# Kernel tuning notes

Hardware: AMD Instinct MI355X
Metric: run time of the kernel (lower is better)

The kernel has to match this reference:

```python
import jax, jax.numpy as jnp
import numpy as np

TOP_K = 2
NUM_MOE_LAYERS = 12


def _gemma_mlp(x, gate_w, up_w, down_w):
    # GemmaMLP: down( gelu_tanh(gate(x)) * up(x) )
    g = jnp.einsum('bsh,hi->bsi', x, gate_w)
    u = jnp.einsum('bsh,hi->bsi', x, up_w)
    return jnp.einsum('bsi,ih->bsh', jax.nn.gelu(g, approximate=True) * u, down_w)


def setup_inputs() -> dict:
    key = jax.random.key(0)
    ks = jax.random.split(key, 8)
    B, S, H, I, E = 32, 256, 1024, 4096, 8  # batch, seq, hidden, intermediate, skill experts
    std = 0.02
    return {
        'x': jax.random.normal(ks[0], (B, S, H), jnp.float32),
        'router_logits': jax.random.normal(ks[1], (B, E), jnp.float32),
        'skill_gate': jax.random.normal(ks[2], (E, H, I), jnp.float32) * std,
        'skill_up': jax.random.normal(ks[3], (E, H, I), jnp.float32) * std,
        'skill_down': jax.random.normal(ks[4], (E, I, H), jnp.float32) * std,
        'shared_gate': jax.random.normal(ks[5], (H, I), jnp.float32) * std,
        'shared_up': jax.random.normal(ks[6], (H, I), jnp.float32) * std,
        'shared_down': jax.random.normal(ks[7], (I, H), jnp.float32) * std,
    }


def reference(x, router_logits, skill_gate, skill_up, skill_down,
              shared_gate, shared_up, shared_down):
    B = x.shape[0]
    E = skill_gate.shape[0]
    # top-k softmax routing (per sequence), renormalized over selected experts
    rw = jax.nn.softmax(router_logits.astype(jnp.float32), axis=-1)
    w, sel = jax.lax.top_k(rw, TOP_K)                      # [B, k]
    w = w / w.sum(axis=-1, keepdims=True)
    w = w.astype(x.dtype)
    # ScaleGradient: identity fwd, grad scaled by 1/num_moe_layers
    scale = 1.0 / NUM_MOE_LAYERS
    w = scale * w + (1.0 - scale) * jax.lax.stop_gradient(w)
    # dense combine weights [B, E]; zero weight == not routed (same math as gather/scatter)
    dense_w = jnp.zeros((B, E), x.dtype).at[jnp.arange(B)[:, None], sel].add(w)

    def step(acc, params):
        g, u, d, we = params                               # we: [B]
        return acc + we[:, None, None] * _gemma_mlp(x, g, u, d), None

    out, _ = jax.lax.scan(step, jnp.zeros_like(x),
                          (skill_gate, skill_up, skill_down, dense_w.T))
    out = out + _gemma_mlp(x, shared_gate, shared_up, shared_down)
    return out
```

## Files before the change

kernel.cpp:

```cpp
#include <hip/hip_runtime.h>

typedef __bf16 bf16x8 __attribute__((ext_vector_type(8)));
typedef float  f32x4  __attribute__((ext_vector_type(4)));

__device__ __forceinline__ unsigned short f2bf(float f) {
    unsigned u = __float_as_uint(f);
    u += 0x7fffu + ((u >> 16) & 1u);
    return (unsigned short)(u >> 16);
}

__device__ __forceinline__ void gld_lds16(const void* g, void* l) {
    __builtin_amdgcn_global_load_lds(
        (const __attribute__((address_space(1))) void*)g,
        (__attribute__((address_space(3))) void*)l,
        16, 0, 0);
}

#define NB  32
#define SQ  256
#define HD  1024
#define ID  4096
#define NEXP 8
#define PAIRS (NB * 3)

#define OFF_EID    ((size_t)0)
#define OFF_WGT    ((size_t)512)
#define OFF_XBF    ((size_t)1024)
#define OFF_GATET  (OFF_XBF   + (size_t)16777216)
#define OFF_UPT    (OFF_GATET + (size_t)75497472)
#define OFF_DOWNT  (OFF_UPT   + (size_t)75497472)
#define OFF_ACT    (OFF_DOWNT + (size_t)75497472)

__global__ void routing_kernel(const float* __restrict__ logits,
                               int* __restrict__ eid, float* __restrict__ wgt) {
    int b = threadIdx.x;
    if (b < NB) {
        float l[NEXP];
        for (int j = 0; j < NEXP; ++j) l[j] = logits[b * NEXP + j];
        int a0 = 0;
        for (int j = 1; j < NEXP; ++j) if (l[j] > l[a0]) a0 = j;
        int a1 = -1;
        for (int j = 0; j < NEXP; ++j) {
            if (j == a0) continue;
            if (a1 < 0 || l[j] > l[a1]) a1 = j;
        }
        float w0 = 1.0f / (1.0f + expf(l[a1] - l[a0]));
        eid[b * 3 + 0] = a0;  wgt[b * 3 + 0] = w0;
        eid[b * 3 + 1] = a1;  wgt[b * 3 + 1] = 1.0f - w0;
        eid[b * 3 + 2] = NEXP; wgt[b * 3 + 2] = 1.0f;
    }
}

__global__ void xcvt_kernel(const float* __restrict__ x,
                            unsigned short* __restrict__ xb, int n4) {
    int i = blockIdx.x * 256 + threadIdx.x;
    if (i < n4) {
        float4 v = ((const float4*)x)[i];
        union { unsigned short s[4]; uint2 u; } p;
        p.s[0] = f2bf(v.x); p.s[1] = f2bf(v.y);
        p.s[2] = f2bf(v.z); p.s[3] = f2bf(v.w);
        ((uint2*)xb)[i] = p.u;
    }
}

__global__ void transpose_cvt(const float* __restrict__ skill,
                              const float* __restrict__ shared_m,
                              unsigned short* __restrict__ out, int R, int C) {
    const int e = blockIdx.z;
    const float* src = (e < NEXP) ? (skill + (size_t)e * R * C) : shared_m;
    unsigned short* dst = out + (size_t)e * R * C;
    const int c0 = blockIdx.x * 64;
    const int r0 = blockIdx.y * 64;
    __shared__ unsigned short t[64][66];
    const int tid = threadIdx.x;
    const int lr = tid >> 4;
    const int lc = (tid & 15) * 4;
    for (int it = 0; it < 4; ++it) {
        int r = lr + it * 16;
        float4 v = *(const float4*)(src + (size_t)(r0 + r) * C + c0 + lc);
        t[r][lc + 0] = f2bf(v.x);
        t[r][lc + 1] = f2bf(v.y);
        t[r][lc + 2] = f2bf(v.z);
        t[r][lc + 3] = f2bf(v.w);
    }
    __syncthreads();
    const int oc = tid >> 2;
    const int k0 = (tid & 3) * 16;
    unsigned int pk[8];
    for (int j = 0; j < 8; ++j) {
        unsigned int lo = t[k0 + 2 * j + 0][oc];
        unsigned int hi = t[k0 + 2 * j + 1][oc];
        pk[j] = lo | (hi << 16);
    }
    unsigned short* dp = dst + (size_t)(c0 + oc) * R + r0 + k0;
    ((uint4*)dp)[0] = make_uint4(pk[0], pk[1], pk[2], pk[3]);
    ((uint4*)dp)[1] = make_uint4(pk[4], pk[5], pk[6], pk[7]);
}

__global__ __launch_bounds__(256, 2) void stage1_gateup(
    const unsigned short* __restrict__ xbf,
    const unsigned short* __restrict__ gateT,
    const unsigned short* __restrict__ upT,
    const int* __restrict__ eid, const float* __restrict__ wgt,
    unsigned short* __restrict__ act)
{
    const int nt = blockIdx.x;
    const int mt = blockIdx.y;
    const int p  = blockIdx.z;
    const int b  = p / 3;
    const int e  = eid[p];
    const float w = wgt[p];

    __shared__ __align__(16) unsigned short lds[3 * 128 * 64];
    unsigned short* La = lds;
    unsigned short* Lg = lds + 8192;
    unsigned short* Lu = lds + 16384;

    const int tid  = threadIdx.x;
    const int wave = tid >> 6;
    const int lane = tid & 63;
    const int wm = (wave >> 1) * 64;
    const int wn = (wave & 1) * 64;

    const unsigned short* Abase = xbf   + (size_t)(b * SQ + mt * 128) * HD;
    const unsigned short* Gbase = gateT + ((size_t)e * ID + nt * 128) * HD;
    const unsigned short* Ubase = upT   + ((size_t)e * ID + nt * 128) * HD;

    const int srow = lane >> 3;
    const int scol = (lane & 7) * 8;

    f32x4 accg[4][4], accu[4][4];
    for (int i = 0; i < 4; ++i)
        for (int j = 0; j < 4; ++j) { accg[i][j] = (f32x4)0.f; accu[i][j] = (f32x4)0.f; }

    const int lrow = lane & 15;
    const int kq   = (lane >> 4) * 8;

    for (int k0 = 0; k0 < HD; k0 += 64) {
        for (int q = 0; q < 4; ++q) {
            const int seg = wave * 4 + q;
            const size_t roff = (size_t)(seg * 8 + srow);
            gld_lds16(Abase + roff * HD + k0 + scol, La + seg * 512);
            gld_lds16(Gbase + roff * HD + k0 + scol, Lg + seg * 512);
            gld_lds16(Ubase + roff * HD + k0 + scol, Lu + seg * 512);
        }
        __syncthreads();
        for (int kk = 0; kk < 64; kk += 32) {
            bf16x8 af[4], gf[4], uf[4];
            for (int mf = 0; mf < 4; ++mf)
                af[mf] = *(const bf16x8*)(La + (wm + mf * 16 + lrow) * 64 + kk + kq);
            for (int nf = 0; nf < 4; ++nf) {
                gf[nf] = *(const bf16x8*)(Lg + (wn + nf * 16 + lrow) * 64 + kk + kq);
                uf[nf] = *(const bf16x8*)(Lu + (wn + nf * 16 + lrow) * 64 + kk + kq);
            }
            for (int mf = 0; mf < 4; ++mf)
                for (int nf = 0; nf < 4; ++nf) {
                    accg[mf][nf] = __builtin_amdgcn_mfma_f32_16x16x32_bf16(af[mf], gf[nf], accg[mf][nf], 0, 0, 0);
                    accu[mf][nf] = __builtin_amdgcn_mfma_f32_16x16x32_bf16(af[mf], uf[nf], accu[mf][nf], 0, 0, 0);
                }
        }
        __syncthreads();
    }

    unsigned short* actp = act + (size_t)p * (SQ * ID);
    const int rb = mt * 128 + wm + ((lane >> 4) << 2);
    const int cb = nt * 128 + wn + (lane & 15);
    for (int mf = 0; mf < 4; ++mf)
        for (int nf = 0; nf < 4; ++nf)
            for (int r = 0; r < 4; ++r) {
                float g = accg[mf][nf][r];
                float u = accu[mf][nf][r];
                float t = 0.7978845608028654f * (g + 0.044715f * g * g * g);
                float h = 0.5f * g * (1.0f + tanhf(t)) * u * w;
                actp[(size_t)(rb + mf * 16 + r) * ID + cb + nf * 16] = f2bf(h);
            }
}

__global__ __launch_bounds__(256, 2) void stage2_down(
    const unsigned short* __restrict__ act,
    const unsigned short* __restrict__ downT,
    const int* __restrict__ eid,
    float* __restrict__ out)
{
    const int nt = blockIdx.x;
    const int mt = blockIdx.y;
    const int b  = blockIdx.z;

    __shared__ __align__(16) unsigned short lds[2 * 128 * 64];
    unsigned short* La = lds;
    unsigned short* Lb = lds + 8192;

    const int tid  = threadIdx.x;
    const int wave = tid >> 6;
    const int lane = tid & 63;
    const int wm = (wave >> 1) * 64;
    const int wn = (wave & 1) * 64;

    const int e0 = eid[b * 3 + 0], e1 = eid[b * 3 + 1], e2 = eid[b * 3 + 2];

    const int srow = lane >> 3;
    const int scol = (lane & 7) * 8;
    const int lrow = lane & 15;
    const int kq   = (lane >> 4) * 8;

    f32x4 acc[4][4];
    for (int i = 0; i < 4; ++i)
        for (int j = 0; j < 4; ++j) acc[i][j] = (f32x4)0.f;

    for (int k0 = 0; k0 < 3 * ID; k0 += 64) {
        const int slot = k0 >> 12;
        const int i0   = k0 & (ID - 1);
        const int e    = (slot == 0) ? e0 : (slot == 1 ? e1 : e2);
        const unsigned short* Abase = act   + ((size_t)(b * 3 + slot) * SQ + mt * 128) * ID + i0;
        const unsigned short* Bbase = downT + ((size_t)e * HD + nt * 128) * ID + i0;
        for (int q = 0; q < 4; ++q) {
            const int seg = wave * 4 + q;
            const size_t roff = (size_t)(seg * 8 + srow);
            gld_lds16(Abase + roff * ID + scol, La + seg * 512);
            gld_lds16(Bbase + roff * ID + scol, Lb + seg * 512);
        }
        __syncthreads();
        for (int kk = 0; kk < 64; kk += 32) {
            bf16x8 af[4], bf[4];
            for (int mf = 0; mf < 4; ++mf)
                af[mf] = *(const bf16x8*)(La + (wm + mf * 16 + lrow) * 64 + kk + kq);
            for (int nf = 0; nf < 4; ++nf)
                bf[nf] = *(const bf16x8*)(Lb + (wn + nf * 16 + lrow) * 64 + kk + kq);
            for (int mf = 0; mf < 4; ++mf)
                for (int nf = 0; nf < 4; ++nf)
                    acc[mf][nf] = __builtin_amdgcn_mfma_f32_16x16x32_bf16(af[mf], bf[nf], acc[mf][nf], 0, 0, 0);
        }
        __syncthreads();
    }

    const int rb = mt * 128 + wm + ((lane >> 4) << 2);
    const int cb = nt * 128 + wn + (lane & 15);
    for (int mf = 0; mf < 4; ++mf)
        for (int nf = 0; nf < 4; ++nf)
            for (int r = 0; r < 4; ++r)
                out[((size_t)b * SQ + rb + mf * 16 + r) * HD + cb + nf * 16] = acc[mf][nf][r];
}

extern "C" void kernel_launch(void* const* d_in, const int* in_sizes, int n_in,
                              void* d_out, int out_size, void* d_ws, size_t ws_size,
                              hipStream_t stream) {
    const float* x        = (const float*)d_in[0];
    const float* logits   = (const float*)d_in[1];
    const float* sk_gate  = (const float*)d_in[2];
    const float* sk_up    = (const float*)d_in[3];
    const float* sk_down  = (const float*)d_in[4];
    const float* sh_gate  = (const float*)d_in[5];
    const float* sh_up    = (const float*)d_in[6];
    const float* sh_down  = (const float*)d_in[7];
    float* out = (float*)d_out;

    char* ws = (char*)d_ws;
    int*            eid   = (int*)(ws + OFF_EID);
    float*          wgt   = (float*)(ws + OFF_WGT);
    unsigned short* xbf   = (unsigned short*)(ws + OFF_XBF);
    unsigned short* gateT = (unsigned short*)(ws + OFF_GATET);
    unsigned short* upT   = (unsigned short*)(ws + OFF_UPT);
    unsigned short* downT = (unsigned short*)(ws + OFF_DOWNT);
    unsigned short* act   = (unsigned short*)(ws + OFF_ACT);

    routing_kernel<<<1, 64, 0, stream>>>(logits, eid, wgt);

    const int n4 = (NB * SQ * HD) / 4;
    xcvt_kernel<<<(n4 + 255) / 256, 256, 0, stream>>>(x, xbf, n4);

    transpose_cvt<<<dim3(ID / 64, HD / 64, 9), 256, 0, stream>>>(sk_gate, sh_gate, gateT, HD, ID);
    transpose_cvt<<<dim3(ID / 64, HD / 64, 9), 256, 0, stream>>>(sk_up,   sh_up,   upT,   HD, ID);
    transpose_cvt<<<dim3(HD / 64, ID / 64, 9), 256, 0, stream>>>(sk_down, sh_down, downT, ID, HD);

    stage1_gateup<<<dim3(ID / 128, SQ / 128, PAIRS), 256, 0, stream>>>(xbf, gateT, upT, eid, wgt, act);
    stage2_down<<<dim3(HD / 128, SQ / 128, NB), 256, 0, stream>>>(act, downT, eid, out);
}
```

Baseline: 1.307 ms.

## Rewrite MoE GEMMs with 256x128 tiles, swizzled LDS, double-buffered prefetch and split-K

Both GEMM kernels become 512-thread blocks. Stage 1 covers the full 256-row sequence per block, fusing the gate and up columns into one B tile. Blocks are ordered by expert through a sort table built in the routing kernel so same-expert tiles share cache. LDS is XOR-swizzled and double-buffered, with explicit vmcnt waits, sched barriers and raised priority around the MFMA bursts, and GELU now uses an exp-based form. Stage 2 uses 256x256 tiles with 2-way split-K into a partial buffer plus a combine kernel, which costs an extra full-output read/write pass in exchange for better occupancy and fewer blocks.

```diff
diff --git a/kernel.cpp b/kernel.cpp
--- a/kernel.cpp
+++ b/kernel.cpp
@@ -15,6 +15,10 @@
         (__attribute__((address_space(3))) void*)l,
         16, 0, 0);
 }
+
+#define WAITVM(N) asm volatile("s_waitcnt vmcnt(" #N ")" ::: "memory")
+#define SB0()     __builtin_amdgcn_sched_barrier(0)
+#define BAR()     __builtin_amdgcn_s_barrier()
 
 #define NB  32
 #define SQ  256
@@ -30,6 +34,8 @@
 #define OFF_UPT    (OFF_GATET + (size_t)75497472)
 #define OFF_DOWNT  (OFF_UPT   + (size_t)75497472)
 #define OFF_ACT    (OFF_DOWNT + (size_t)75497472)
+
+__device__ int d_sord[PAIRS];
 
 __global__ void routing_kernel(const float* __restrict__ logits,
                                int* __restrict__ eid, float* __restrict__ wgt) {
@@ -48,6 +54,14 @@
         eid[b * 3 + 0] = a0;  wgt[b * 3 + 0] = w0;
         eid[b * 3 + 1] = a1;  wgt[b * 3 + 1] = 1.0f - w0;
         eid[b * 3 + 2] = NEXP; wgt[b * 3 + 2] = 1.0f;
+    }
+    __syncthreads();
+    if (threadIdx.x == 0) {
+        int cnt[NEXP + 2];
+        for (int i = 0; i < NEXP + 2; ++i) cnt[i] = 0;
+        for (int i = 0; i < PAIRS; ++i) cnt[eid[i] + 1]++;
+        for (int e = 0; e < NEXP + 1; ++e) cnt[e + 1] += cnt[e];
+        for (int i = 0; i < PAIRS; ++i) d_sord[cnt[eid[i]]++] = i;
     }
 }
 
@@ -97,148 +111,273 @@
     ((uint4*)dp)[1] = make_uint4(pk[4], pk[5], pk[6], pk[7]);
 }
 
-__global__ __launch_bounds__(256, 2) void stage1_gateup(
+#define LDFRAGS(KH, MB)                                                      \
+    _Pragma("unroll") for (int i2 = 0; i2 < 4; ++i2)                         \
+        av[i2] = *(const bf16x8*)(Lc + (KH) + rdA + ((MB) + i2) * 512);
+#define LDBFRAGS(KH)                                                         \
+    _Pragma("unroll") for (int i2 = 0; i2 < 4; ++i2)                         \
+        bv[i2] = *(const bf16x8*)(Lc + (KH) + rdB + i2 * 512);
+#define DOMFMA(MB)                                                           \
+    __builtin_amdgcn_s_setprio(1);                                           \
+    _Pragma("unroll") for (int mi = 0; mi < 4; ++mi)                         \
+        _Pragma("unroll") for (int ni = 0; ni < 4; ++ni)                     \
+            acc[(MB) + mi][ni] = __builtin_amdgcn_mfma_f32_16x16x32_bf16(    \
+                av[mi], bv[ni], acc[(MB) + mi][ni], 0, 0, 0);                \
+    __builtin_amdgcn_s_setprio(0);
+
+__global__ __launch_bounds__(512, 2) void stage1_gateup(
     const unsigned short* __restrict__ xbf,
     const unsigned short* __restrict__ gateT,
     const unsigned short* __restrict__ upT,
     const int* __restrict__ eid, const float* __restrict__ wgt,
     unsigned short* __restrict__ act)
 {
-    const int nt = blockIdx.x;
-    const int mt = blockIdx.y;
-    const int p  = blockIdx.z;
-    const int b  = p / 3;
-    const int e  = eid[p];
-    const float w = wgt[p];
-
-    __shared__ __align__(16) unsigned short lds[3 * 128 * 64];
-    unsigned short* La = lds;
-    unsigned short* Lg = lds + 8192;
-    unsigned short* Lu = lds + 16384;
+    extern __shared__ unsigned short lds[];
+
+    const int bid = blockIdx.x;
+    const int g   = bid & 7;
+    const int r0_ = bid >> 3;
+    const int sg  = r0_ >> 7;
+    const int rr  = r0_ & 127;
+    const int nt  = rr >> 2;
+    const int pi  = rr & 3;
+    const int p   = d_sord[g * 12 + sg * 4 + pi];
+    const int b   = p / 3;
+    const int e   = eid[p];
+    const float wS = wgt[p];
 
     const int tid  = threadIdx.x;
-    const int wave = tid >> 6;
+    const int wv   = tid >> 6;
     const int lane = tid & 63;
-    const int wm = (wave >> 1) * 64;
-    const int wn = (wave & 1) * 64;
-
-    const unsigned short* Abase = xbf   + (size_t)(b * SQ + mt * 128) * HD;
-    const unsigned short* Gbase = gateT + ((size_t)e * ID + nt * 128) * HD;
-    const unsigned short* Ubase = upT   + ((size_t)e * ID + nt * 128) * HD;
-
-    const int srow = lane >> 3;
-    const int scol = (lane & 7) * 8;
-
-    f32x4 accg[4][4], accu[4][4];
-    for (int i = 0; i < 4; ++i)
-        for (int j = 0; j < 4; ++j) { accg[i][j] = (f32x4)0.f; accu[i][j] = (f32x4)0.f; }
-
+    const int wr   = wv >> 2;
+    const int wc   = wv & 3;
     const int lrow = lane & 15;
-    const int kq   = (lane >> 4) * 8;
-
-    for (int k0 = 0; k0 < HD; k0 += 64) {
-        for (int q = 0; q < 4; ++q) {
-            const int seg = wave * 4 + q;
-            const size_t roff = (size_t)(seg * 8 + srow);
-            gld_lds16(Abase + roff * HD + k0 + scol, La + seg * 512);
-            gld_lds16(Gbase + roff * HD + k0 + scol, Lg + seg * 512);
-            gld_lds16(Ubase + roff * HD + k0 + scol, Lu + seg * 512);
+    const int chunk = lane >> 4;
+    const int lr4  = lane >> 2;
+
+    const int stc8 = (((lane & 3) ^ ((lane >> 2) & 3)) << 3);
+    const int dA   = (wv * 2) * 512;
+
+    const unsigned short* pa[2];
+    const unsigned short* pb[2];
+#pragma unroll
+    for (int q = 0; q < 2; ++q) {
+        const int seg = wv * 2 + q;
+        pa[q] = xbf + ((size_t)(b * SQ + seg * 16 + lr4)) * HD + stc8;
+        const int s    = (seg >> 1) & 1;
+        const int icol = nt * 128 + (seg >> 2) * 32 + (seg & 1) * 16 + lr4;
+        pb[q] = (s ? upT : gateT) + ((size_t)e * ID + icol) * HD + stc8;
+    }
+
+    const int rdA = (wr * 128 + lrow) * 32 + ((chunk ^ (lrow & 3)) << 3);
+    const int rdB = 16384 + (wc * 64 + lrow) * 32 + ((chunk ^ (lrow & 3)) << 3);
+
+    f32x4 acc[8][4];
+#pragma unroll
+    for (int i = 0; i < 8; ++i)
+#pragma unroll
+        for (int j = 0; j < 4; ++j) acc[i][j] = (f32x4)0.f;
+
+    {
+        unsigned short* L0 = lds;
+        gld_lds16(pa[0],      L0 +          dA);
+        gld_lds16(pa[1],      L0 +          dA + 512);
+        gld_lds16(pb[0],      L0 + 16384 +  dA);
+        gld_lds16(pb[1],      L0 + 16384 +  dA + 512);
+        gld_lds16(pa[0] + 32, L0 +  8192 +  dA);
+        gld_lds16(pa[1] + 32, L0 +  8192 +  dA + 512);
+        gld_lds16(pb[0] + 32, L0 + 24576 +  dA);
+        gld_lds16(pb[1] + 32, L0 + 24576 +  dA + 512);
+        SB0(); WAITVM(4); SB0();
+        BAR();
+    }
+
+    const int NT = HD / 64;
+#pragma unroll 1
+    for (int t = 0; t < NT; ++t) {
+        unsigned short* Lc = lds + (t & 1) * 32768;
+        unsigned short* Ln = lds + ((t & 1) ^ 1) * 32768;
+        const bool pf = (t + 1 < NT);
+        const int kof = (t + 1) * 64;
+        bf16x8 av[4], bv[4];
+
+        LDFRAGS(0, 0); LDBFRAGS(0);
+        if (pf) { gld_lds16(pa[0] + kof, Ln + dA); gld_lds16(pa[1] + kof, Ln + dA + 512); }
+        BAR();
+        DOMFMA(0);
+        BAR();
+
+        LDFRAGS(0, 4);
+        if (pf) { gld_lds16(pb[0] + kof, Ln + 16384 + dA); gld_lds16(pb[1] + kof, Ln + 16384 + dA + 512); }
+        SB0();
+        if (pf) { WAITVM(4); } else { WAITVM(0); }
+        SB0();
+        BAR();
+        DOMFMA(4);
+        BAR();
+
+        LDFRAGS(8192, 0); LDBFRAGS(8192);
+        if (pf) { gld_lds16(pa[0] + kof + 32, Ln + 8192 + dA); gld_lds16(pa[1] + kof + 32, Ln + 8192 + dA + 512); }
+        BAR();
+        DOMFMA(0);
+        BAR();
+
+        LDFRAGS(8192, 4);
+        if (pf) {
+            gld_lds16(pb[0] + kof + 32, Ln + 24576 + dA);
+            gld_lds16(pb[1] + kof + 32, Ln + 24576 + dA + 512);
+            SB0(); WAITVM(4); SB0();
         }
-        __syncthreads();
-        for (int kk = 0; kk < 64; kk += 32) {
-            bf16x8 af[4], gf[4], uf[4];
-            for (int mf = 0; mf < 4; ++mf)
-                af[mf] = *(const bf16x8*)(La + (wm + mf * 16 + lrow) * 64 + kk + kq);
-            for (int nf = 0; nf < 4; ++nf) {
-                gf[nf] = *(const bf16x8*)(Lg + (wn + nf * 16 + lrow) * 64 + kk + kq);
-                uf[nf] = *(const bf16x8*)(Lu + (wn + nf * 16 + lrow) * 64 + kk + kq);
+        BAR();
+        DOMFMA(4);
+        BAR();
+    }
+
+    unsigned short* actp = act + (size_t)p * (SQ * ID);
+    const int rb = wr * 128 + (chunk << 2);
+    const int cb = nt * 128 + wc * 32 + lrow;
+#pragma unroll
+    for (int mf = 0; mf < 8; ++mf)
+#pragma unroll
+        for (int pp = 0; pp < 2; ++pp)
+#pragma unroll
+            for (int r2 = 0; r2 < 4; ++r2) {
+                float gv = acc[mf][pp][r2];
+                float uv = acc[mf][pp + 2][r2];
+                float t2 = -1.5957691216057308f * gv * (1.0f + 0.044715f * gv * gv);
+                float h  = __fdividef(gv, 1.0f + __expf(t2)) * uv * wS;
+                actp[(size_t)(rb + mf * 16 + r2) * ID + cb + pp * 16] = f2bf(h);
             }
-            for (int mf = 0; mf < 4; ++mf)
-                for (int nf = 0; nf < 4; ++nf) {
-                    accg[mf][nf] = __builtin_amdgcn_mfma_f32_16x16x32_bf16(af[mf], gf[nf], accg[mf][nf], 0, 0, 0);
-                    accu[mf][nf] = __builtin_amdgcn_mfma_f32_16x16x32_bf16(af[mf], uf[nf], accu[mf][nf], 0, 0, 0);
-                }
-        }
-        __syncthreads();
-    }
-
-    unsigned short* actp = act + (size_t)p * (SQ * ID);
-    const int rb = mt * 128 + wm + ((lane >> 4) << 2);
-    const int cb = nt * 128 + wn + (lane & 15);
-    for (int mf = 0; mf < 4; ++mf)
-        for (int nf = 0; nf < 4; ++nf)
-            for (int r = 0; r < 4; ++r) {
-                float g = accg[mf][nf][r];
-                float u = accu[mf][nf][r];
-                float t = 0.7978845608028654f * (g + 0.044715f * g * g * g);
-                float h = 0.5f * g * (1.0f + tanhf(t)) * u * w;
-                actp[(size_t)(rb + mf * 16 + r) * ID + cb + nf * 16] = f2bf(h);
-            }
-}
-
-__global__ __launch_bounds__(256, 2) void stage2_down(
+}
+
+__global__ __launch_bounds__(512, 2) void stage2_down(
     const unsigned short* __restrict__ act,
     const unsigned short* __restrict__ downT,
     const int* __restrict__ eid,
-    float* __restrict__ out)
+    float* __restrict__ out,
+    float* __restrict__ part1)
 {
-    const int nt = blockIdx.x;
-    const int mt = blockIdx.y;
-    const int b  = blockIdx.z;
-
-    __shared__ __align__(16) unsigned short lds[2 * 128 * 64];
-    unsigned short* La = lds;
-    unsigned short* Lb = lds + 8192;
+    extern __shared__ unsigned short lds[];
+
+    const int lid = blockIdx.x;
+    const int sw  = (lid & 7) * 32 + (lid >> 3);
+    const int z   = sw >> 7;
+    const int q7  = sw & 127;
+    const int b   = q7 >> 2;
+    const int ntH = q7 & 3;
+    const int b3  = b * 3;
+    const int e0 = eid[b3], e1 = eid[b3 + 1], e2 = eid[b3 + 2];
 
     const int tid  = threadIdx.x;
-    const int wave = tid >> 6;
+    const int wv   = tid >> 6;
     const int lane = tid & 63;
-    const int wm = (wave >> 1) * 64;
-    const int wn = (wave & 1) * 64;
-
-    const int e0 = eid[b * 3 + 0], e1 = eid[b * 3 + 1], e2 = eid[b * 3 + 2];
-
-    const int srow = lane >> 3;
-    const int scol = (lane & 7) * 8;
+    const int wr   = wv >> 2;
+    const int wc   = wv & 3;
     const int lrow = lane & 15;
-    const int kq   = (lane >> 4) * 8;
-
-    f32x4 acc[4][4];
-    for (int i = 0; i < 4; ++i)
+    const int chunk = lane >> 4;
+    const int lr4  = lane >> 2;
+    const int stc8 = (((lane & 3) ^ ((lane >> 2) & 3)) << 3);
+    const int dA   = (wv * 2) * 512;
+
+    const int rdA = (wr * 128 + lrow) * 32 + ((chunk ^ (lrow & 3)) << 3);
+    const int rdB = 16384 + (wc * 64 + lrow) * 32 + ((chunk ^ (lrow & 3)) << 3);
+
+    f32x4 acc[8][4];
+#pragma unroll
+    for (int i = 0; i < 8; ++i)
+#pragma unroll
         for (int j = 0; j < 4; ++j) acc[i][j] = (f32x4)0.f;
 
-    for (int k0 = 0; k0 < 3 * ID; k0 += 64) {
-        const int slot = k0 >> 12;
-        const int i0   = k0 & (ID - 1);
-        const int e    = (slot == 0) ? e0 : (slot == 1 ? e1 : e2);
-        const unsigned short* Abase = act   + ((size_t)(b * 3 + slot) * SQ + mt * 128) * ID + i0;
-        const unsigned short* Bbase = downT + ((size_t)e * HD + nt * 128) * ID + i0;
-        for (int q = 0; q < 4; ++q) {
-            const int seg = wave * 4 + q;
-            const size_t roff = (size_t)(seg * 8 + srow);
-            gld_lds16(Abase + roff * ID + scol, La + seg * 512);
-            gld_lds16(Bbase + roff * ID + scol, Lb + seg * 512);
+    auto mksrc = [&](int gk, const unsigned short*& a0, const unsigned short*& a1,
+                     const unsigned short*& b0, const unsigned short*& b1) {
+        const int slot = gk >> 6;
+        const int i0   = (gk & 63) << 6;
+        const int esl  = (slot == 0) ? e0 : ((slot == 1) ? e1 : e2);
+        a0 = act + ((size_t)((b3 + slot) * SQ) + wv * 32 + lr4) * ID + i0 + stc8;
+        a1 = a0 + (size_t)16 * ID;
+        b0 = downT + ((size_t)esl * HD + ntH * 256 + wv * 32 + lr4) * ID + i0 + stc8;
+        b1 = b0 + (size_t)16 * ID;
+    };
+
+    {
+        const unsigned short *a0, *a1, *b0, *b1;
+        mksrc(z * 96, a0, a1, b0, b1);
+        unsigned short* L0 = lds;
+        gld_lds16(a0,      L0 +          dA);
+        gld_lds16(a1,      L0 +          dA + 512);
+        gld_lds16(b0,      L0 + 16384 +  dA);
+        gld_lds16(b1,      L0 + 16384 +  dA + 512);
+        gld_lds16(a0 + 32, L0 +  8192 +  dA);
+        gld_lds16(a1 + 32, L0 +  8192 +  dA + 512);
+        gld_lds16(b0 + 32, L0 + 24576 +  dA);
+        gld_lds16(b1 + 32, L0 + 24576 +  dA + 512);
+        SB0(); WAITVM(4); SB0();
+        BAR();
+    }
+
+    const int NT = 96;
+#pragma unroll 1
+    for (int t = 0; t < NT; ++t) {
+        unsigned short* Lc = lds + (t & 1) * 32768;
+        unsigned short* Ln = lds + ((t & 1) ^ 1) * 32768;
+        const bool pf = (t + 1 < NT);
+        const unsigned short *a0 = nullptr, *a1 = nullptr, *b0 = nullptr, *b1 = nullptr;
+        if (pf) mksrc(z * 96 + t + 1, a0, a1, b0, b1);
+        bf16x8 av[4], bv[4];
+
+        LDFRAGS(0, 0); LDBFRAGS(0);
+        if (pf) { gld_lds16(a0, Ln + dA); gld_lds16(a1, Ln + dA + 512); }
+        BAR();
+        DOMFMA(0);
+        BAR();
+
+        LDFRAGS(0, 4);
+        if (pf) { gld_lds16(b0, Ln + 16384 + dA); gld_lds16(b1, Ln + 16384 + dA + 512); }
+        SB0();
+        if (pf) { WAITVM(4); } else { WAITVM(0); }
+        SB0();
+        BAR();
+        DOMFMA(4);
+        BAR();
+
+        LDFRAGS(8192, 0); LDBFRAGS(8192);
+        if (pf) { gld_lds16(a0 + 32, Ln + 8192 + dA); gld_lds16(a1 + 32, Ln + 8192 + dA + 512); }
+        BAR();
+        DOMFMA(0);
+        BAR();
+
+        LDFRAGS(8192, 4);
+        if (pf) {
+            gld_lds16(b0 + 32, Ln + 24576 + dA);
+            gld_lds16(b1 + 32, Ln + 24576 + dA + 512);
+            SB0(); WAITVM(4); SB0();
         }
-        __syncthreads();
-        for (int kk = 0; kk < 64; kk += 32) {
-            bf16x8 af[4], bf[4];
-            for (int mf = 0; mf < 4; ++mf)
-                af[mf] = *(const bf16x8*)(La + (wm + mf * 16 + lrow) * 64 + kk + kq);
-            for (int nf = 0; nf < 4; ++nf)
-                bf[nf] = *(const bf16x8*)(Lb + (wn + nf * 16 + lrow) * 64 + kk + kq);
-            for (int mf = 0; mf < 4; ++mf)
-                for (int nf = 0; nf < 4; ++nf)
-                    acc[mf][nf] = __builtin_amdgcn_mfma_f32_16x16x32_bf16(af[mf], bf[nf], acc[mf][nf], 0, 0, 0);
-        }
-        __syncthreads();
-    }
-
-    const int rb = mt * 128 + wm + ((lane >> 4) << 2);
-    const int cb = nt * 128 + wn + (lane & 15);
-    for (int mf = 0; mf < 4; ++mf)
+        BAR();
+        DOMFMA(4);
+        BAR();
+    }
+
+    float* dst = (z == 0) ? out : part1;
+    const int rb = wr * 128 + (chunk << 2);
+    const int cb = ntH * 256 + wc * 64 + lrow;
+#pragma unroll
+    for (int mf = 0; mf < 8; ++mf)
+#pragma unroll
         for (int nf = 0; nf < 4; ++nf)
-            for (int r = 0; r < 4; ++r)
-                out[((size_t)b * SQ + rb + mf * 16 + r) * HD + cb + nf * 16] = acc[mf][nf][r];
+#pragma unroll
+            for (int r2 = 0; r2 < 4; ++r2)
+                dst[((size_t)b * SQ + rb + mf * 16 + r2) * HD + cb + nf * 16] = acc[mf][nf][r2];
+}
+
+__global__ void combine_kernel(float* __restrict__ out,
+                               const float* __restrict__ p1, int n4) {
+    int i = blockIdx.x * 256 + threadIdx.x;
+    if (i < n4) {
+        float4 a = ((const float4*)out)[i];
+        float4 c = ((const float4*)p1)[i];
+        a.x += c.x; a.y += c.y; a.z += c.z; a.w += c.w;
+        ((float4*)out)[i] = a;
+    }
 }
 
 extern "C" void kernel_launch(void* const* d_in, const int* in_sizes, int n_in,
@@ -262,6 +401,16 @@
     unsigned short* upT   = (unsigned short*)(ws + OFF_UPT);
     unsigned short* downT = (unsigned short*)(ws + OFF_DOWNT);
     unsigned short* act   = (unsigned short*)(ws + OFF_ACT);
+    float*          part1 = (float*)(ws + OFF_GATET);
+
+    static int attr_set = 0;
+    if (!attr_set) {
+        hipFuncSetAttribute(reinterpret_cast<const void*>(stage1_gateup),
+                            hipFuncAttributeMaxDynamicSharedMemorySize, 131072);
+        hipFuncSetAttribute(reinterpret_cast<const void*>(stage2_down),
+                            hipFuncAttributeMaxDynamicSharedMemorySize, 131072);
+        attr_set = 1;
+    }
 
     routing_kernel<<<1, 64, 0, stream>>>(logits, eid, wgt);
 
@@ -272,6 +421,9 @@
     transpose_cvt<<<dim3(ID / 64, HD / 64, 9), 256, 0, stream>>>(sk_up,   sh_up,   upT,   HD, ID);
     transpose_cvt<<<dim3(HD / 64, ID / 64, 9), 256, 0, stream>>>(sk_down, sh_down, downT, ID, HD);
 
-    stage1_gateup<<<dim3(ID / 128, SQ / 128, PAIRS), 256, 0, stream>>>(xbf, gateT, upT, eid, wgt, act);
-    stage2_down<<<dim3(HD / 128, SQ / 128, NB), 256, 0, stream>>>(act, downT, eid, out);
-}
+    stage1_gateup<<<dim3(PAIRS * 32), 512, 131072, stream>>>(xbf, gateT, upT, eid, wgt, act);
+    stage2_down<<<dim3(256), 512, 131072, stream>>>(act, downT, eid, out, part1);
+
+    const int c4 = (NB * SQ * HD) / 4;
+    combine_kernel<<<(c4 + 255) / 256, 256, 0, stream>>>(out, part1, c4);
+}
```

Result: faster. 1.125 ms (-13.9%).
